# Kernel optimization log

Hardware: AMD Instinct MI355X
Metric: run time of the kernel (lower is better)

## Reference

```python
import jax, jax.numpy as jnp
import numpy as np

L, D, DFF, H, B, S = 6, 1024, 4096, 16, 4, 512
DK = D // H
EPS = 1e-6


def setup_inputs() -> dict:
    key = jax.random.key(0)
    ks = jax.random.split(key, 20)
    sc = 0.02
    n = jax.random.normal
    return {
        "x": n(ks[0], (B, S, D), jnp.float32),
        "Wq": n(ks[1], (L, D, D)) * sc, "bq": jnp.zeros((L, D)),
        "Wk": n(ks[2], (L, D, D)) * sc, "bk": jnp.zeros((L, D)),
        "Wv": n(ks[3], (L, D, D)) * sc, "bv": jnp.zeros((L, D)),
        "Wo": n(ks[4], (L, D, D)) * sc, "bo": jnp.zeros((L, D)),
        "W1": n(ks[5], (L, D, DFF)) * sc, "b1": jnp.zeros((L, DFF)),
        "W2": n(ks[6], (L, DFF, D)) * sc, "b2": jnp.zeros((L, D)),
        "ln1_a": jnp.ones((L, D)), "ln1_b": jnp.zeros((L, D)),
        "ln2_a": jnp.ones((L, D)), "ln2_b": jnp.zeros((L, D)),
        "norm_a": jnp.ones((D,)), "norm_b": jnp.zeros((D,)),
    }


def _ln(x, a, b):
    # custom LayerNorm: uses sample std (ddof=1, like torch.std) and (std + eps)
    m = x.mean(-1, keepdims=True)
    s = jnp.std(x, axis=-1, ddof=1, keepdims=True)
    return a * (x - m) / (s + EPS) + b


def reference(x, Wq, bq, Wk, bk, Wv, bv, Wo, bo, W1, b1, W2, b2,
              ln1_a, ln1_b, ln2_a, ln2_b, norm_a, norm_b):
    inv = 1.0 / jnp.sqrt(jnp.float32(DK))
    for l in range(L):
        # --- self-attention sublayer (pre-norm, residual) ---
        h = _ln(x, ln1_a[l], ln1_b[l])
        q = (h @ Wq[l] + bq[l]).reshape(B, S, H, DK)
        k = (h @ Wk[l] + bk[l]).reshape(B, S, H, DK)
        v = (h @ Wv[l] + bv[l]).reshape(B, S, H, DK)
        scores = jnp.einsum('bqhd,bkhd->bhqk', q, k) * inv
        p = jax.nn.softmax(scores, axis=-1)
        o = jnp.einsum('bhqk,bkhd->bqhd', p, v).reshape(B, S, D)
        x = x + (o @ Wo[l] + bo[l])
        # --- feed-forward sublayer ---
        h = _ln(x, ln2_a[l], ln2_b[l])
        x = x + (jax.nn.relu(h @ W1[l] + b1[l]) @ W2[l] + b2[l])
    return _ln(x, norm_a, norm_b)
```

## Files before the change

kernel.cpp:

```cpp
#include <hip/hip_runtime.h>
#include <hip/hip_bf16.h>

typedef __hip_bfloat16 bf16;
typedef __bf16 bf16x8 __attribute__((ext_vector_type(8)));
typedef float f32x4 __attribute__((ext_vector_type(4)));

static constexpr int L_ = 6, D_ = 1024, DFF_ = 4096, H_ = 16, B_ = 4, S_ = 512, DK_ = 64;
static constexpr int N_ = B_ * S_;

#define GLOAD_LDS(gp, lp) __builtin_amdgcn_global_load_lds( \
    (const __attribute__((address_space(1))) void*)(gp),    \
    (__attribute__((address_space(3))) void*)(lp), 16, 0, 0)

__global__ void transpose_cast(const float* __restrict__ in, bf16* __restrict__ out,
                               int K, int M, long zin, long zout) {
    const float* ip = in + (size_t)blockIdx.z * zin;
    bf16* op = out + (size_t)blockIdx.z * zout;
    __shared__ float t[32][33];
    int m0 = blockIdx.x * 32, k0 = blockIdx.y * 32;
    int tx = threadIdx.x, ty = threadIdx.y;
    #pragma unroll
    for (int i = 0; i < 32; i += 8)
        t[ty + i][tx] = ip[(size_t)(k0 + ty + i) * M + m0 + tx];
    __syncthreads();
    #pragma unroll
    for (int i = 0; i < 32; i += 8)
        op[(size_t)(m0 + ty + i) * K + k0 + tx] = __float2bfloat16(t[tx][ty + i]);
}

__global__ void pack_qkv_bias(const float* __restrict__ bq, const float* __restrict__ bk,
                              const float* __restrict__ bv, float* __restrict__ out) {
    int t = blockIdx.x * 256 + threadIdx.x;
    int l = t / (3 * D_), c = t % (3 * D_);
    float v = c < D_ ? bq[l * D_ + c] : (c < 2 * D_ ? bk[l * D_ + c - D_] : bv[l * D_ + c - 2 * D_]);
    out[t] = v;
}

template <typename OutT>
__global__ __launch_bounds__(256) void ln_kernel(const float* __restrict__ x,
                                                 const float* __restrict__ ga,
                                                 const float* __restrict__ gb,
                                                 OutT* __restrict__ out) {
    int row = blockIdx.x;
    float4 v = ((const float4*)(x + (size_t)row * D_))[threadIdx.x];
    float s = v.x + v.y + v.z + v.w;
    float q = v.x * v.x + v.y * v.y + v.z * v.z + v.w * v.w;
    #pragma unroll
    for (int m = 1; m < 64; m <<= 1) { s += __shfl_xor(s, m, 64); q += __shfl_xor(q, m, 64); }
    __shared__ float ps[4], pq[4];
    int wid = threadIdx.x >> 6;
    if ((threadIdx.x & 63) == 0) { ps[wid] = s; pq[wid] = q; }
    __syncthreads();
    s = ps[0] + ps[1] + ps[2] + ps[3];
    q = pq[0] + pq[1] + pq[2] + pq[3];
    float mean = s * (1.0f / D_);
    float var = (q - (float)D_ * mean * mean) * (1.0f / (D_ - 1));
    var = var < 0.f ? 0.f : var;
    float rstd = 1.0f / (sqrtf(var) + 1e-6f);
    int c = threadIdx.x * 4;
    float xv[4] = {v.x, v.y, v.z, v.w};
    #pragma unroll
    for (int r = 0; r < 4; r++) {
        float o = ga[c + r] * (xv[r] - mean) * rstd + gb[c + r];
        if constexpr (__hip_internal::is_same<OutT, float>::value)
            out[(size_t)row * D_ + c + r] = o;
        else
            out[(size_t)row * D_ + c + r] = __float2bfloat16(o);
    }
}

__global__ __launch_bounds__(256) void softmax_kernel(bf16* __restrict__ sc) {
    int wrow = blockIdx.x * 4 + (threadIdx.x >> 6);
    int lane = threadIdx.x & 63;
    bf16* rp = sc + (size_t)wrow * S_ + lane * 8;
    ushort4 u0 = *(const ushort4*)rp;
    ushort4 u1 = *(const ushort4*)(rp + 4);
    float f[8];
    f[0] = __uint_as_float((unsigned)u0.x << 16);
    f[1] = __uint_as_float((unsigned)u0.y << 16);
    f[2] = __uint_as_float((unsigned)u0.z << 16);
    f[3] = __uint_as_float((unsigned)u0.w << 16);
    f[4] = __uint_as_float((unsigned)u1.x << 16);
    f[5] = __uint_as_float((unsigned)u1.y << 16);
    f[6] = __uint_as_float((unsigned)u1.z << 16);
    f[7] = __uint_as_float((unsigned)u1.w << 16);
    float mx = f[0];
    #pragma unroll
    for (int i = 1; i < 8; i++) mx = fmaxf(mx, f[i]);
    #pragma unroll
    for (int m = 1; m < 64; m <<= 1) mx = fmaxf(mx, __shfl_xor(mx, m, 64));
    float sum = 0.f;
    #pragma unroll
    for (int i = 0; i < 8; i++) { f[i] = __expf(f[i] - mx); sum += f[i]; }
    #pragma unroll
    for (int m = 1; m < 64; m <<= 1) sum += __shfl_xor(sum, m, 64);
    float r = 1.0f / sum;
    #pragma unroll
    for (int i = 0; i < 8; i++) rp[i] = __float2bfloat16(f[i] * r);
}

__device__ inline void swz_tiles(int& ntile, int& mtile) {
    unsigned o = blockIdx.y * gridDim.x + blockIdx.x;
    if (gridDim.z == 1) {
        unsigned nwg = gridDim.x * gridDim.y;
        unsigned q = nwg >> 3, r = nwg & 7;
        unsigned xcd = o & 7, j = o >> 3;
        o = (xcd < r ? xcd * (q + 1) : r * (q + 1) + (xcd - r) * q) + j;
    }
    ntile = o % gridDim.x;
    mtile = o / gridDim.x;
}

enum { EPI_SCALE = 0, EPI_RELU = 2, EPI_RESID = 3 };

template <int BM, int BN, int EPI>
__global__ __launch_bounds__(256) void gemm_bt(
    const bf16* __restrict__ A, int lda, long sAb, long sAh,
    const bf16* __restrict__ Bt, int ldb, long sBb, long sBh,
    const float* __restrict__ bias,
    void* __restrict__ Cv, int ldc, long sCb, long sCh,
    int K, float alpha) {
    constexpr int BK = 32;
    constexpr int WM = BM / 2, WN = BN / 2;
    constexpr int FM = WM / 16, FN = WN / 16;
    constexpr int IA = (BM * BK) / 512 / 4;
    constexpr int IB = (BN * BK) / 512 / 4;
    __shared__ __align__(16) bf16 As[BM * BK];
    __shared__ __align__(16) bf16 Bs[BN * BK];
    const int tid = threadIdx.x, wid = tid >> 6, lane = tid & 63;
    const int bb = blockIdx.z >> 4, hh = blockIdx.z & 15;
    A += (size_t)bb * sAb + (size_t)hh * sAh;
    Bt += (size_t)bb * sBb + (size_t)hh * sBh;
    int ntile, mtile;
    swz_tiles(ntile, mtile);
    const int m0 = mtile * BM, n0 = ntile * BN;
    const int wm = (wid >> 1) * WM, wn = (wid & 1) * WN;
    const int srow = lane >> 2, skk = 8 * (lane & 3);
    const int fr = lane & 15, fg = lane >> 4;
    f32x4 acc[FM][FN] = {};
    for (int k0 = 0; k0 < K; k0 += BK) {
        __syncthreads();
        #pragma unroll
        for (int i = 0; i < IA; i++) {
            int inst = wid * IA + i;
            const bf16* gp = A + (size_t)(m0 + inst * 16 + srow) * lda + k0 + skk;
            GLOAD_LDS(gp, &As[inst * 512]);
        }
        #pragma unroll
        for (int i = 0; i < IB; i++) {
            int inst = wid * IB + i;
            const bf16* gp = Bt + (size_t)(n0 + inst * 16 + srow) * ldb + k0 + skk;
            GLOAD_LDS(gp, &Bs[inst * 512]);
        }
        __syncthreads();
        bf16x8 af[FM], bfr[FN];
        #pragma unroll
        for (int i = 0; i < FM; i++)
            af[i] = *(const bf16x8*)&As[(wm + i * 16 + fr) * BK + 8 * fg];
        #pragma unroll
        for (int j = 0; j < FN; j++)
            bfr[j] = *(const bf16x8*)&Bs[(wn + j * 16 + fr) * BK + 8 * fg];
        #pragma unroll
        for (int i = 0; i < FM; i++)
            #pragma unroll
            for (int j = 0; j < FN; j++)
                acc[i][j] = __builtin_amdgcn_mfma_f32_16x16x32_bf16(af[i], bfr[j], acc[i][j], 0, 0, 0);
    }
    #pragma unroll
    for (int i = 0; i < FM; i++) {
        #pragma unroll
        for (int j = 0; j < FN; j++) {
            int rr = m0 + wm + i * 16 + (lane >> 4) * 4;
            int cc = n0 + wn + j * 16 + (lane & 15);
            float bv = 0.f;
            if constexpr (EPI == EPI_RELU || EPI == EPI_RESID) bv = bias[cc];
            #pragma unroll
            for (int r = 0; r < 4; r++) {
                float v = acc[i][j][r];
                if constexpr (EPI == EPI_SCALE) {
                    bf16* C = (bf16*)Cv + (size_t)bb * sCb + (size_t)hh * sCh;
                    C[(size_t)(rr + r) * ldc + cc] = __float2bfloat16(v * alpha);
                } else if constexpr (EPI == EPI_RELU) {
                    bf16* C = (bf16*)Cv;
                    float o = v + bv;
                    C[(size_t)(rr + r) * ldc + cc] = __float2bfloat16(o > 0.f ? o : 0.f);
                } else {
                    float* C = (float*)Cv;
                    C[(size_t)(rr + r) * ldc + cc] += v + bv;
                }
            }
        }
    }
}

__global__ __launch_bounds__(256) void gemm_qkv(
    const bf16* __restrict__ A, const bf16* __restrict__ Bt, const float* __restrict__ bias,
    bf16* __restrict__ qb, bf16* __restrict__ kb, bf16* __restrict__ vT) {
    constexpr int BM = 64, BN = 128, BK = 32;
    constexpr int WM = 32, WN = 64, FM = 2, FN = 4;
    __shared__ __align__(16) bf16 As[BM * BK];
    __shared__ __align__(16) bf16 Bs[BN * BK];
    const int tid = threadIdx.x, wid = tid >> 6, lane = tid & 63;
    int ntile, mtile;
    swz_tiles(ntile, mtile);
    const int m0 = mtile * BM, n0 = ntile * BN;
    const int wm = (wid >> 1) * WM, wn = (wid & 1) * WN;
    const int srow = lane >> 2, skk = 8 * (lane & 3);
    const int fr = lane & 15, fg = lane >> 4;
    f32x4 acc[FM][FN] = {};
    for (int k0 = 0; k0 < D_; k0 += BK) {
        __syncthreads();
        {
            const bf16* gp = A + (size_t)(m0 + wid * 16 + srow) * D_ + k0 + skk;
            GLOAD_LDS(gp, &As[wid * 512]);
        }
        #pragma unroll
        for (int i = 0; i < 2; i++) {
            int inst = wid * 2 + i;
            const bf16* gp = Bt + (size_t)(n0 + inst * 16 + srow) * D_ + k0 + skk;
            GLOAD_LDS(gp, &Bs[inst * 512]);
        }
        __syncthreads();
        bf16x8 af[FM], bfr[FN];
        #pragma unroll
        for (int i = 0; i < FM; i++)
            af[i] = *(const bf16x8*)&As[(wm + i * 16 + fr) * BK + 8 * fg];
        #pragma unroll
        for (int j = 0; j < FN; j++)
            bfr[j] = *(const bf16x8*)&Bs[(wn + j * 16 + fr) * BK + 8 * fg];
        #pragma unroll
        for (int i = 0; i < FM; i++)
            #pragma unroll
            for (int j = 0; j < FN; j++)
                acc[i][j] = __builtin_amdgcn_mfma_f32_16x16x32_bf16(af[i], bfr[j], acc[i][j], 0, 0, 0);
    }
    #pragma unroll
    for (int i = 0; i < FM; i++) {
        #pragma unroll
        for (int j = 0; j < FN; j++) {
            int rr = m0 + wm + i * 16 + (lane >> 4) * 4;
            int cc = n0 + wn + j * 16 + (lane & 15);
            float bv = bias[cc];
            #pragma unroll
            for (int r = 0; r < 4; r++) {
                float v = acc[i][j][r] + bv;
                if (cc < D_) {
                    qb[(size_t)(rr + r) * D_ + cc] = __float2bfloat16(v);
                } else if (cc < 2 * D_) {
                    kb[(size_t)(rr + r) * D_ + cc - D_] = __float2bfloat16(v);
                } else {
                    vT[((size_t)(rr >> 9) * D_ + cc - 2 * D_) * S_ + ((rr & 511) + r)] = __float2bfloat16(v);
                }
            }
        }
    }
}

extern "C" void kernel_launch(void* const* d_in, const int* in_sizes, int n_in,
                              void* d_out, int out_size, void* d_ws, size_t ws_size,
                              hipStream_t stream) {
    (void)in_sizes; (void)n_in; (void)out_size;
    const float* x    = (const float*)d_in[0];
    const float* Wq   = (const float*)d_in[1];
    const float* pbq  = (const float*)d_in[2];
    const float* Wk   = (const float*)d_in[3];
    const float* pbk  = (const float*)d_in[4];
    const float* Wv   = (const float*)d_in[5];
    const float* pbv  = (const float*)d_in[6];
    const float* Wo   = (const float*)d_in[7];
    const float* pbo  = (const float*)d_in[8];
    const float* W1   = (const float*)d_in[9];
    const float* pb1  = (const float*)d_in[10];
    const float* W2   = (const float*)d_in[11];
    const float* pb2  = (const float*)d_in[12];
    const float* l1a  = (const float*)d_in[13];
    const float* l1b  = (const float*)d_in[14];
    const float* l2a  = (const float*)d_in[15];
    const float* l2b  = (const float*)d_in[16];
    const float* nrma = (const float*)d_in[17];
    const float* nrmb = (const float*)d_in[18];

    char* ws = (char*)d_ws;
    size_t off = 0;
    auto alloc = [&](size_t bytes) { void* p = ws + off; off += (bytes + 255) & ~(size_t)255; return p; };
    float* xf  = (float*)alloc((size_t)N_ * D_ * 4);
    bf16* hbuf = (bf16*)alloc((size_t)N_ * D_ * 2);
    bf16* qbuf = (bf16*)alloc((size_t)N_ * D_ * 2);
    bf16* kbuf = (bf16*)alloc((size_t)N_ * D_ * 2);
    bf16* vT   = (bf16*)alloc((size_t)B_ * D_ * S_ * 2);
    bf16* obuf = (bf16*)alloc((size_t)N_ * D_ * 2);
    float* qkvb = (float*)alloc((size_t)L_ * 3 * D_ * 4);
    size_t scElems = (size_t)B_ * H_ * S_ * S_;
    size_t midElems = (size_t)N_ * DFF_;
    bf16* sc   = (bf16*)alloc((scElems > midElems ? scElems : midElems) * 2);
    bf16* mid  = sc;
    const size_t szDD = (size_t)D_ * D_, szDF = (size_t)D_ * DFF_;
    size_t wtFull = (3 * L_ * szDD + L_ * szDD + 2 * L_ * szDF) * 2;
    size_t wtLayer = (4 * szDD + 2 * szDF) * 2;
    bool full = (off + wtFull) <= ws_size;
    bf16* WT = (bf16*)alloc(full ? wtFull : wtLayer);

    pack_qkv_bias<<<L_ * 3 * D_ / 256, 256, 0, stream>>>(pbq, pbk, pbv, qkvb);

    bf16 *Wqkv0, *WoT0, *W1T0, *W2T0;
    dim3 tb(32, 8);
    if (full) {
        Wqkv0 = WT;
        WoT0  = WT + 3 * L_ * szDD;
        W1T0  = WoT0 + L_ * szDD;
        W2T0  = W1T0 + L_ * szDF;
        transpose_cast<<<dim3(D_ / 32, D_ / 32, L_), tb, 0, stream>>>(Wq, Wqkv0, D_, D_, szDD, 3 * szDD);
        transpose_cast<<<dim3(D_ / 32, D_ / 32, L_), tb, 0, stream>>>(Wk, Wqkv0 + szDD, D_, D_, szDD, 3 * szDD);
        transpose_cast<<<dim3(D_ / 32, D_ / 32, L_), tb, 0, stream>>>(Wv, Wqkv0 + 2 * szDD, D_, D_, szDD, 3 * szDD);
        transpose_cast<<<dim3(D_ / 32, D_ / 32, L_), tb, 0, stream>>>(Wo, WoT0, D_, D_, szDD, szDD);
        transpose_cast<<<dim3(DFF_ / 32, D_ / 32, L_), tb, 0, stream>>>(W1, W1T0, D_, DFF_, szDF, szDF);
        transpose_cast<<<dim3(D_ / 32, DFF_ / 32, L_), tb, 0, stream>>>(W2, W2T0, DFF_, D_, szDF, szDF);
    } else {
        Wqkv0 = WT; WoT0 = WT + 3 * szDD; W1T0 = WoT0 + szDD; W2T0 = W1T0 + szDF;
    }

    hipMemcpyAsync(xf, x, (size_t)N_ * D_ * 4, hipMemcpyDeviceToDevice, stream);

    const long SD = (long)S_ * D_, HSS = (long)H_ * S_ * S_, SSq = (long)S_ * S_;
    const long DS = (long)D_ * S_, DKS = (long)DK_ * S_;

    for (int l = 0; l < L_; l++) {
        const bf16 *WqkvT, *WoT, *W1T, *W2T;
        if (full) {
            WqkvT = Wqkv0 + (size_t)l * 3 * szDD;
            WoT = WoT0 + l * szDD; W1T = W1T0 + l * szDF; W2T = W2T0 + l * szDF;
        } else {
            transpose_cast<<<dim3(D_ / 32, D_ / 32, 1), tb, 0, stream>>>(Wq + l * szDD, Wqkv0, D_, D_, 0, 0);
            transpose_cast<<<dim3(D_ / 32, D_ / 32, 1), tb, 0, stream>>>(Wk + l * szDD, Wqkv0 + szDD, D_, D_, 0, 0);
            transpose_cast<<<dim3(D_ / 32, D_ / 32, 1), tb, 0, stream>>>(Wv + l * szDD, Wqkv0 + 2 * szDD, D_, D_, 0, 0);
            transpose_cast<<<dim3(D_ / 32, D_ / 32, 1), tb, 0, stream>>>(Wo + l * szDD, WT + 3 * szDD, D_, D_, 0, 0);
            transpose_cast<<<dim3(DFF_ / 32, D_ / 32, 1), tb, 0, stream>>>(W1 + l * szDF, W1T0, D_, DFF_, 0, 0);
            transpose_cast<<<dim3(D_ / 32, DFF_ / 32, 1), tb, 0, stream>>>(W2 + l * szDF, W2T0, DFF_, D_, 0, 0);
            WqkvT = Wqkv0; WoT = WoT0; W1T = W1T0; W2T = W2T0;
        }

        ln_kernel<bf16><<<N_, 256, 0, stream>>>(xf, l1a + l * D_, l1b + l * D_, hbuf);
        gemm_qkv<<<dim3(3 * D_ / 128, N_ / 64, 1), 256, 0, stream>>>(
            hbuf, WqkvT, qkvb + (size_t)l * 3 * D_, qbuf, kbuf, vT);
        gemm_bt<128, 128, EPI_SCALE><<<dim3(S_ / 128, S_ / 128, B_ * H_), 256, 0, stream>>>(
            qbuf, D_, SD, DK_, kbuf, D_, SD, DK_, nullptr, sc, S_, HSS, SSq, DK_, 0.125f);
        softmax_kernel<<<B_ * H_ * S_ / 4, 256, 0, stream>>>(sc);
        gemm_bt<64, 64, EPI_SCALE><<<dim3(DK_ / 64, S_ / 64, B_ * H_), 256, 0, stream>>>(
            sc, S_, HSS, SSq, vT, S_, DS, DKS, nullptr, obuf, D_, SD, DK_, S_, 1.f);
        gemm_bt<64, 64, EPI_RESID><<<dim3(D_ / 64, N_ / 64, 1), 256, 0, stream>>>(
            obuf, D_, 0, 0, WoT, D_, 0, 0, pbo + l * D_, xf, D_, 0, 0, D_, 1.f);

        ln_kernel<bf16><<<N_, 256, 0, stream>>>(xf, l2a + l * D_, l2b + l * D_, hbuf);
        gemm_bt<64, 128, EPI_RELU><<<dim3(DFF_ / 128, N_ / 64, 1), 256, 0, stream>>>(
            hbuf, D_, 0, 0, W1T, D_, 0, 0, pb1 + l * DFF_, mid, DFF_, 0, 0, D_, 1.f);
        gemm_bt<64, 64, EPI_RESID><<<dim3(D_ / 64, N_ / 64, 1), 256, 0, stream>>>(
            mid, DFF_, 0, 0, W2T, DFF_, 0, 0, pb2 + l * D_, xf, D_, 0, 0, DFF_, 1.f);
    }

    ln_kernel<float><<<N_, 256, 0, stream>>>(xf, nrma, nrmb, (float*)d_out);
}
```

Baseline: 1.204 ms.

## Enlarge GEMM tiles to 128x128 and add split-K atomic residual GEMMs

Grows the output tiles of the QKV, FFN1 and attention-PV GEMMs so each tile reuses more data, which leaves fewer workgroups per launch. The Wo and W2 residual GEMMs move to 128x128 tiles with split-K of 2 and 4, writing into the residual buffer with float atomics, so the launch still has enough workgroups. This trades repeated operand loads for atomic traffic and makes the summation order nondeterministic. It also fixes the Wo transpose destination pointer on the non-full path.

```diff
diff --git a/kernel.cpp b/kernel.cpp
--- a/kernel.cpp
+++ b/kernel.cpp
@@ -111,9 +111,9 @@
     mtile = o / gridDim.x;
 }
 
-enum { EPI_SCALE = 0, EPI_RELU = 2, EPI_RESID = 3 };
-
-template <int BM, int BN, int EPI>
+enum { EPI_SCALE = 0, EPI_RELU = 2, EPI_RESID = 3, EPI_ATOMIC = 4 };
+
+template <int BM, int BN, int EPI, int SPLITK = 1>
 __global__ __launch_bounds__(256) void gemm_bt(
     const bf16* __restrict__ A, int lda, long sAb, long sAh,
     const bf16* __restrict__ Bt, int ldb, long sBb, long sBh,
@@ -128,17 +128,24 @@
     __shared__ __align__(16) bf16 As[BM * BK];
     __shared__ __align__(16) bf16 Bs[BN * BK];
     const int tid = threadIdx.x, wid = tid >> 6, lane = tid & 63;
-    const int bb = blockIdx.z >> 4, hh = blockIdx.z & 15;
-    A += (size_t)bb * sAb + (size_t)hh * sAh;
-    Bt += (size_t)bb * sBb + (size_t)hh * sBh;
+    int bb = 0, hh = 0, kz = 0;
+    if constexpr (SPLITK > 1) {
+        kz = blockIdx.z;
+    } else {
+        bb = blockIdx.z >> 4; hh = blockIdx.z & 15;
+        A += (size_t)bb * sAb + (size_t)hh * sAh;
+        Bt += (size_t)bb * sBb + (size_t)hh * sBh;
+    }
     int ntile, mtile;
     swz_tiles(ntile, mtile);
     const int m0 = mtile * BM, n0 = ntile * BN;
     const int wm = (wid >> 1) * WM, wn = (wid & 1) * WN;
     const int srow = lane >> 2, skk = 8 * (lane & 3);
     const int fr = lane & 15, fg = lane >> 4;
+    const int Kc = K / SPLITK;
+    const int kbeg = kz * Kc, kend = kbeg + Kc;
     f32x4 acc[FM][FN] = {};
-    for (int k0 = 0; k0 < K; k0 += BK) {
+    for (int k0 = kbeg; k0 < kend; k0 += BK) {
         __syncthreads();
         #pragma unroll
         for (int i = 0; i < IA; i++) {
@@ -173,7 +180,7 @@
             int rr = m0 + wm + i * 16 + (lane >> 4) * 4;
             int cc = n0 + wn + j * 16 + (lane & 15);
             float bv = 0.f;
-            if constexpr (EPI == EPI_RELU || EPI == EPI_RESID) bv = bias[cc];
+            if constexpr (EPI == EPI_RELU || EPI == EPI_RESID || EPI == EPI_ATOMIC) bv = bias[cc];
             #pragma unroll
             for (int r = 0; r < 4; r++) {
                 float v = acc[i][j][r];
@@ -184,9 +191,12 @@
                     bf16* C = (bf16*)Cv;
                     float o = v + bv;
                     C[(size_t)(rr + r) * ldc + cc] = __float2bfloat16(o > 0.f ? o : 0.f);
+                } else if constexpr (EPI == EPI_RESID) {
+                    float* C = (float*)Cv;
+                    C[(size_t)(rr + r) * ldc + cc] += v + bv;
                 } else {
                     float* C = (float*)Cv;
-                    C[(size_t)(rr + r) * ldc + cc] += v + bv;
+                    atomicAdd(&C[(size_t)(rr + r) * ldc + cc], v + (kz == 0 ? bv : 0.f));
                 }
             }
         }
@@ -196,8 +206,8 @@
 __global__ __launch_bounds__(256) void gemm_qkv(
     const bf16* __restrict__ A, const bf16* __restrict__ Bt, const float* __restrict__ bias,
     bf16* __restrict__ qb, bf16* __restrict__ kb, bf16* __restrict__ vT) {
-    constexpr int BM = 64, BN = 128, BK = 32;
-    constexpr int WM = 32, WN = 64, FM = 2, FN = 4;
+    constexpr int BM = 128, BN = 128, BK = 32;
+    constexpr int WM = 64, WN = 64, FM = 4, FN = 4;
     __shared__ __align__(16) bf16 As[BM * BK];
     __shared__ __align__(16) bf16 Bs[BN * BK];
     const int tid = threadIdx.x, wid = tid >> 6, lane = tid & 63;
@@ -210,9 +220,11 @@
     f32x4 acc[FM][FN] = {};
     for (int k0 = 0; k0 < D_; k0 += BK) {
         __syncthreads();
-        {
-            const bf16* gp = A + (size_t)(m0 + wid * 16 + srow) * D_ + k0 + skk;
-            GLOAD_LDS(gp, &As[wid * 512]);
+        #pragma unroll
+        for (int i = 0; i < 2; i++) {
+            int inst = wid * 2 + i;
+            const bf16* gp = A + (size_t)(m0 + inst * 16 + srow) * D_ + k0 + skk;
+            GLOAD_LDS(gp, &As[inst * 512]);
         }
         #pragma unroll
         for (int i = 0; i < 2; i++) {
@@ -333,27 +345,27 @@
             transpose_cast<<<dim3(D_ / 32, D_ / 32, 1), tb, 0, stream>>>(Wq + l * szDD, Wqkv0, D_, D_, 0, 0);
             transpose_cast<<<dim3(D_ / 32, D_ / 32, 1), tb, 0, stream>>>(Wk + l * szDD, Wqkv0 + szDD, D_, D_, 0, 0);
             transpose_cast<<<dim3(D_ / 32, D_ / 32, 1), tb, 0, stream>>>(Wv + l * szDD, Wqkv0 + 2 * szDD, D_, D_, 0, 0);
-            transpose_cast<<<dim3(D_ / 32, D_ / 32, 1), tb, 0, stream>>>(Wo + l * szDD, WT + 3 * szDD, D_, D_, 0, 0);
+            transpose_cast<<<dim3(D_ / 32, D_ / 32, 1), tb, 0, stream>>>(Wo + l * szDD, WoT0, D_, D_, 0, 0);
             transpose_cast<<<dim3(DFF_ / 32, D_ / 32, 1), tb, 0, stream>>>(W1 + l * szDF, W1T0, D_, DFF_, 0, 0);
             transpose_cast<<<dim3(D_ / 32, DFF_ / 32, 1), tb, 0, stream>>>(W2 + l * szDF, W2T0, DFF_, D_, 0, 0);
             WqkvT = Wqkv0; WoT = WoT0; W1T = W1T0; W2T = W2T0;
         }
 
         ln_kernel<bf16><<<N_, 256, 0, stream>>>(xf, l1a + l * D_, l1b + l * D_, hbuf);
-        gemm_qkv<<<dim3(3 * D_ / 128, N_ / 64, 1), 256, 0, stream>>>(
+        gemm_qkv<<<dim3(3 * D_ / 128, N_ / 128, 1), 256, 0, stream>>>(
             hbuf, WqkvT, qkvb + (size_t)l * 3 * D_, qbuf, kbuf, vT);
         gemm_bt<128, 128, EPI_SCALE><<<dim3(S_ / 128, S_ / 128, B_ * H_), 256, 0, stream>>>(
             qbuf, D_, SD, DK_, kbuf, D_, SD, DK_, nullptr, sc, S_, HSS, SSq, DK_, 0.125f);
         softmax_kernel<<<B_ * H_ * S_ / 4, 256, 0, stream>>>(sc);
-        gemm_bt<64, 64, EPI_SCALE><<<dim3(DK_ / 64, S_ / 64, B_ * H_), 256, 0, stream>>>(
+        gemm_bt<128, 64, EPI_SCALE><<<dim3(DK_ / 64, S_ / 128, B_ * H_), 256, 0, stream>>>(
             sc, S_, HSS, SSq, vT, S_, DS, DKS, nullptr, obuf, D_, SD, DK_, S_, 1.f);
-        gemm_bt<64, 64, EPI_RESID><<<dim3(D_ / 64, N_ / 64, 1), 256, 0, stream>>>(
+        gemm_bt<128, 128, EPI_ATOMIC, 2><<<dim3(D_ / 128, N_ / 128, 2), 256, 0, stream>>>(
             obuf, D_, 0, 0, WoT, D_, 0, 0, pbo + l * D_, xf, D_, 0, 0, D_, 1.f);
 
         ln_kernel<bf16><<<N_, 256, 0, stream>>>(xf, l2a + l * D_, l2b + l * D_, hbuf);
-        gemm_bt<64, 128, EPI_RELU><<<dim3(DFF_ / 128, N_ / 64, 1), 256, 0, stream>>>(
+        gemm_bt<128, 128, EPI_RELU><<<dim3(DFF_ / 128, N_ / 128, 1), 256, 0, stream>>>(
             hbuf, D_, 0, 0, W1T, D_, 0, 0, pb1 + l * DFF_, mid, DFF_, 0, 0, D_, 1.f);
-        gemm_bt<64, 64, EPI_RESID><<<dim3(D_ / 64, N_ / 64, 1), 256, 0, stream>>>(
+        gemm_bt<128, 128, EPI_ATOMIC, 4><<<dim3(D_ / 128, N_ / 128, 4), 256, 0, stream>>>(
             mid, DFF_, 0, 0, W2T, DFF_, 0, 0, pb2 + l * D_, xf, D_, 0, 0, DFF_, 1.f);
     }
 
```

Result: slower. 1.283 ms (+6.5%).
